# Kernel optimization log

Measured on AMD Instinct MI355X. Metric: run time of the kernel, lower is better.

The kernel has to match this reference:

```python
import jax, jax.numpy as jnp
import numpy as np

DIM = 512
HIDDEN = 1024
H2 = HIDDEN // 2
B = 384


def setup_inputs() -> dict:
    key = jax.random.key(0)
    ks = jax.random.split(key, 10)
    s_in = 1.0 / np.sqrt(DIM)
    s_h = 1.0 / np.sqrt(H2)
    return {
        "x_samples": jax.random.normal(ks[0], (B, DIM), dtype=jnp.float32),
        "y_samples": jax.random.normal(ks[1], (B, DIM), dtype=jnp.float32),
        "w1_mu": jax.random.uniform(ks[2], (DIM, H2), jnp.float32, -s_in, s_in),
        "b1_mu": jax.random.uniform(ks[3], (H2,), jnp.float32, -s_in, s_in),
        "w2_mu": jax.random.uniform(ks[4], (H2, DIM), jnp.float32, -s_h, s_h),
        "b2_mu": jax.random.uniform(ks[5], (DIM,), jnp.float32, -s_h, s_h),
        "w1_lv": jax.random.uniform(ks[6], (DIM, H2), jnp.float32, -s_in, s_in),
        "b1_lv": jax.random.uniform(ks[7], (H2,), jnp.float32, -s_in, s_in),
        "w2_lv": jax.random.uniform(ks[8], (H2, DIM), jnp.float32, -s_h, s_h),
        "b2_lv": jax.random.uniform(ks[9], (DIM,), jnp.float32, -s_h, s_h),
    }


def reference(x_samples, y_samples, w1_mu, b1_mu, w2_mu, b2_mu,
              w1_lv, b1_lv, w2_lv, b2_lv):
    batch_size = y_samples.shape[0]
    # p_mu / p_logvar MLPs
    mu = jax.nn.relu(x_samples @ w1_mu + b1_mu) @ w2_mu + b2_mu           # [B, D]
    logvar = jnp.tanh(jax.nn.relu(x_samples @ w1_lv + b1_lv) @ w2_lv + b2_lv)  # [B, D]
    inv_var = jnp.exp(-logvar)

    # positive log-likelihood per sample
    positive = (-(mu - y_samples) ** 2 * 0.5 * inv_var - logvar * 0.5).sum(-1)  # [B]

    # pairwise Gaussian log-likelihoods: all_probs[i, j] = log N(y_j; mu_i)
    diff = y_samples[None, :, :] - mu[:, None, :]                          # [B, B, D]
    all_probs = (-diff ** 2 * 0.5 * inv_var[:, None, :]
                 - logvar[:, None, :] * 0.5).sum(-1)                       # [B, B]

    # faithful to the torch broadcast: [B,B] + [B,B,1] -> [B,B,B]
    diag_mask = jnp.eye(batch_size, dtype=jnp.float32)[:, :, None] * -20.0  # [B, B, 1]
    scores = all_probs + diag_mask                                         # [B, B, B]
    negative = jax.scipy.special.logsumexp(scores, axis=0) - jnp.log(batch_size - 1.0)  # [B, B]

    upper = (positive - negative).mean()

    loglikeli = (-(mu - y_samples) ** 2 * inv_var - logvar).sum(1).mean(0)
    return loglikeli + jax.lax.stop_gradient(-loglikeli + upper)
```

## Files before the change

### kernel.cpp

```cpp
#include <hip/hip_runtime.h>
#include <math.h>

#define DIM  512
#define H2   512
#define BSZ  384



template<bool RELU>
__device__ __forceinline__ void gemm_tile(
    const float* __restrict__ A, const float* __restrict__ B,
    const float* __restrict__ bias, float* __restrict__ C,
    int m0, int n0,
    float (*As)[34], float (*Bs)[64])
{
    const int tid = threadIdx.x;
    const int tx = tid & 15;
    const int ty = tid >> 4;

    const int r_a  = tid >> 3;
    const int kg_a = tid & 7;
    const int kr_b = tid >> 4;
    const int cg_b = tid & 15;

    float acc[2][4] = {};

    float4 a_pf  = *(const float4*)&A[(size_t)(m0 + r_a) * 512 + kg_a * 4];
    float4 b_pf0 = *(const float4*)&B[(size_t)kr_b        * 512 + n0 + cg_b * 4];
    float4 b_pf1 = *(const float4*)&B[(size_t)(kr_b + 16) * 512 + n0 + cg_b * 4];

    for (int it = 0; it < 16; ++it) {
        __syncthreads();
        {
            float av[4];
            *(float4*)av = a_pf;
            #pragma unroll
            for (int j = 0; j < 4; ++j) As[kg_a * 4 + j][r_a] = av[j];
            *(float4*)&Bs[kr_b][cg_b * 4]      = b_pf0;
            *(float4*)&Bs[kr_b + 16][cg_b * 4] = b_pf1;
        }
        __syncthreads();

        if (it < 15) {
            const int k0n = (it + 1) * 32;
            a_pf  = *(const float4*)&A[(size_t)(m0 + r_a) * 512 + k0n + kg_a * 4];
            b_pf0 = *(const float4*)&B[(size_t)(k0n + kr_b)      * 512 + n0 + cg_b * 4];
            b_pf1 = *(const float4*)&B[(size_t)(k0n + kr_b + 16) * 512 + n0 + cg_b * 4];
        }

        #pragma unroll
        for (int kk = 0; kk < 32; ++kk) {
            const float a0 = As[kk][ty * 2 + 0];
            const float a1 = As[kk][ty * 2 + 1];
            const float4 bv = *(const float4*)&Bs[kk][tx * 4];
            acc[0][0] += a0 * bv.x; acc[0][1] += a0 * bv.y;
            acc[0][2] += a0 * bv.z; acc[0][3] += a0 * bv.w;
            acc[1][0] += a1 * bv.x; acc[1][1] += a1 * bv.y;
            acc[1][2] += a1 * bv.z; acc[1][3] += a1 * bv.w;
        }
    }

    float bb[4] = {0.f, 0.f, 0.f, 0.f};
    if (RELU) *(float4*)bb = *(const float4*)&bias[n0 + tx * 4];
    #pragma unroll
    for (int i = 0; i < 2; ++i) {
        float4 o;
        if (RELU) {
            o.x = fmaxf(acc[i][0] + bb[0], 0.f);
            o.y = fmaxf(acc[i][1] + bb[1], 0.f);
            o.z = fmaxf(acc[i][2] + bb[2], 0.f);
            o.w = fmaxf(acc[i][3] + bb[3], 0.f);
        } else {
            o.x = acc[i][0]; o.y = acc[i][1]; o.z = acc[i][2]; o.w = acc[i][3];
        }
        *(float4*)&C[(size_t)(m0 + ty * 2 + i) * 512 + n0 + tx * 4] = o;
    }
}

__global__ __launch_bounds__(256) void k_layer1(
    const float* __restrict__ x,
    const float* __restrict__ w1mu, const float* __restrict__ b1mu,
    const float* __restrict__ w1lv, const float* __restrict__ b1lv,
    const float* __restrict__ y,
    float* __restrict__ hmu, float* __restrict__ hlv,
    float* __restrict__ m1p, float* __restrict__ m2p)
{
    __shared__ float As[32][34];
    __shared__ float Bs[32][64];

    const int b = blockIdx.x;
    const int tid = threadIdx.x;

    if (b >= 192) {
        __shared__ float r1[2][512];
        __shared__ float r2[2][512];
        const int sb = b - 192;
        const int c4 = tid & 127;
        const int rh = tid >> 7;
        const int r0 = sb * 64 + rh * 32;
        float s1[4] = {0.f, 0.f, 0.f, 0.f};
        float s2[4] = {0.f, 0.f, 0.f, 0.f};
        for (int r = 0; r < 32; ++r) {
            float v[4];
            *(float4*)v = *(const float4*)&y[(size_t)(r0 + r) * 512 + c4 * 4];
            #pragma unroll
            for (int j = 0; j < 4; ++j) { s1[j] += v[j]; s2[j] += v[j] * v[j]; }
        }
        #pragma unroll
        for (int j = 0; j < 4; ++j) { r1[rh][c4 * 4 + j] = s1[j]; r2[rh][c4 * 4 + j] = s2[j]; }
        __syncthreads();
        if (rh == 0) {
            float4 o1, o2;
            o1.x = s1[0] + r1[1][c4 * 4 + 0]; o1.y = s1[1] + r1[1][c4 * 4 + 1];
            o1.z = s1[2] + r1[1][c4 * 4 + 2]; o1.w = s1[3] + r1[1][c4 * 4 + 3];
            o2.x = s2[0] + r2[1][c4 * 4 + 0]; o2.y = s2[1] + r2[1][c4 * 4 + 1];
            o2.z = s2[2] + r2[1][c4 * 4 + 2]; o2.w = s2[3] + r2[1][c4 * 4 + 3];
            *(float4*)&m1p[sb * 512 + c4 * 4] = o1;
            *(float4*)&m2p[sb * 512 + c4 * 4] = o2;
        }
        return;
    }

    const int branch = b >> 7 >= 1 ? 1 : (b >= 96 ? 1 : 0);
    const int idx = branch ? b - 96 : b;
    const int m0 = (idx >> 3) * 32;
    const int n0 = (idx & 7) * 64;

    if (branch == 0)
        gemm_tile<true>(x, w1mu, b1mu, hmu, m0, n0, As, Bs);
    else
        gemm_tile<true>(x, w1lv, b1lv, hlv, m0, n0, As, Bs);
}

__global__ __launch_bounds__(256) void k_layer2(
    const float* __restrict__ hmu, const float* __restrict__ hlv,
    const float* __restrict__ w2mu, const float* __restrict__ w2lv,
    float* __restrict__ gmu, float* __restrict__ glv)
{
    __shared__ float As[32][34];
    __shared__ float Bs[32][64];

    const int b = blockIdx.x;
    const int branch = b >= 96 ? 1 : 0;
    const int idx = branch ? b - 96 : b;
    const int m0 = (idx >> 3) * 32;
    const int n0 = (idx & 7) * 64;

    if (branch == 0)
        gemm_tile<false>(hmu, w2mu, nullptr, gmu, m0, n0, As, Bs);
    else
        gemm_tile<false>(hlv, w2lv, nullptr, glv, m0, n0, As, Bs);
}

__global__ __launch_bounds__(256) void k_epilogue(
    const float* __restrict__ gmu, const float* __restrict__ glv,
    const float* __restrict__ b2mu, const float* __restrict__ b2lv,
    const float* __restrict__ y,
    const float* __restrict__ m1p, const float* __restrict__ m2p,
    double* __restrict__ partials)
{
    __shared__ double wsum[4];
    const int tid = threadIdx.x;
    const float inv_b = 1.0f / (float)BSZ;

    float tsum = 0.f;
    #pragma unroll
    for (int jj = 0; jj < 2; ++jj) {
        const int e4 = blockIdx.x * 512 + tid * 2 + jj;
        const int col4 = e4 & 127;
        const size_t off = (size_t)e4 * 4;

        float gm[4], gl[4], yv[4], bm[4], bl[4], s1[4], s2[4];
        *(float4*)gm = *(const float4*)&gmu[off];
        *(float4*)gl = *(const float4*)&glv[off];
        *(float4*)yv = *(const float4*)&y[off];
        *(float4*)bm = *(const float4*)&b2mu[col4 * 4];
        *(float4*)bl = *(const float4*)&b2lv[col4 * 4];
        #pragma unroll
        for (int j = 0; j < 4; ++j) { s1[j] = 0.f; s2[j] = 0.f; }
        #pragma unroll
        for (int t = 0; t < 6; ++t) {
            float p1[4], p2[4];
            *(float4*)p1 = *(const float4*)&m1p[t * 512 + col4 * 4];
            *(float4*)p2 = *(const float4*)&m2p[t * 512 + col4 * 4];
            #pragma unroll
            for (int j = 0; j < 4; ++j) { s1[j] += p1[j]; s2[j] += p2[j]; }
        }
        #pragma unroll
        for (int j = 0; j < 4; ++j) {
            const float m1 = s1[j] * inv_b;
            const float m2 = s2[j] * inv_b;
            const float mu = gm[j] + bm[j];
            const float lv = tanhf(gl[j] + bl[j]);
            const float iv = expf(-lv);
            tsum += iv * ((yv[j] * yv[j] - m2) + 2.f * mu * (m1 - yv[j]));
        }
    }

    float s = tsum;
    #pragma unroll
    for (int off = 32; off > 0; off >>= 1) s += __shfl_down(s, off);
    if ((tid & 63) == 0) wsum[tid >> 6] = (double)s;
    __syncthreads();
    if (tid == 0)
        partials[blockIdx.x] = wsum[0] + wsum[1] + wsum[2] + wsum[3];
}

__global__ void k_final(const double* __restrict__ partials, float* __restrict__ out)
{
    const int t = threadIdx.x;
    double v = partials[t] + (t < 32 ? partials[64 + t] : 0.0);
    #pragma unroll
    for (int off = 32; off > 0; off >>= 1) v += __shfl_down(v, off);
    if (t == 0) {
        const double C0 = 5.381602146862063e-12;
        out[0] = (float)(-0.5 * v / (double)BSZ - C0);
    }
}

extern "C" void kernel_launch(void* const* d_in, const int* in_sizes, int n_in,
                              void* d_out, int out_size, void* d_ws, size_t ws_size,
                              hipStream_t stream) {
    const float* x    = (const float*)d_in[0];
    const float* y    = (const float*)d_in[1];
    const float* w1mu = (const float*)d_in[2];
    const float* b1mu = (const float*)d_in[3];
    const float* w2mu = (const float*)d_in[4];
    const float* b2mu = (const float*)d_in[5];
    const float* w1lv = (const float*)d_in[6];
    const float* b1lv = (const float*)d_in[7];
    const float* w2lv = (const float*)d_in[8];
    const float* b2lv = (const float*)d_in[9];
    float* out = (float*)d_out;

    float* ws = (float*)d_ws;
    float* hmu = ws;
    float* hlv = ws + 196608;
    float* gmu = ws + 393216;
    float* glv = ws + 589824;
    float* m1p = ws + 786432;
    float* m2p = ws + 789504;
    double* partials = (double*)(ws + 792576);

    k_layer1<<<198, 256, 0, stream>>>(x, w1mu, b1mu, w1lv, b1lv, y,
                                      hmu, hlv, m1p, m2p);
    k_layer2<<<192, 256, 0, stream>>>(hmu, hlv, w2mu, w2lv, gmu, glv);
    k_epilogue<<<96, 256, 0, stream>>>(gmu, glv, b2mu, b2lv, y, m1p, m2p, partials);
    k_final<<<1, 64, 0, stream>>>(partials, out);
}
```

Measured before the change: 111.8 us.

## Split GEMM K-dimension across blocks and fuse final reduction into epilogue

Both MLP GEMMs now split the K dimension into two halves computed by separate blocks, which doubles the grid to 384 blocks of 128 threads, each producing a 32x64 tile with a 4x4 register tile. The partial results are combined downstream. Layer 2 sums the two layer-1 partials, adds the bias and applies ReLU when loading A, and the epilogue sums the two layer-2 partials. The separate final-reduction kernel is replaced by an atomic counter so the last epilogue block does the reduction, removing one launch. The cost is extra workspace traffic for the partial buffers and a counter reset inside layer1.

```diff
diff --git a/kernel.cpp b/kernel.cpp
--- a/kernel.cpp
+++ b/kernel.cpp
@@ -1,220 +1,238 @@
 #include <hip/hip_runtime.h>
 #include <math.h>
 
-#define DIM  512
-#define H2   512
-#define BSZ  384
-
-
-
-template<bool RELU>
-__device__ __forceinline__ void gemm_tile(
-    const float* __restrict__ A, const float* __restrict__ B,
-    const float* __restrict__ bias, float* __restrict__ C,
-    int m0, int n0,
-    float (*As)[34], float (*Bs)[64])
-{
-    const int tid = threadIdx.x;
-    const int tx = tid & 15;
-    const int ty = tid >> 4;
-
-    const int r_a  = tid >> 3;
-    const int kg_a = tid & 7;
-    const int kr_b = tid >> 4;
-    const int cg_b = tid & 15;
-
-    float acc[2][4] = {};
-
-    float4 a_pf  = *(const float4*)&A[(size_t)(m0 + r_a) * 512 + kg_a * 4];
-    float4 b_pf0 = *(const float4*)&B[(size_t)kr_b        * 512 + n0 + cg_b * 4];
-    float4 b_pf1 = *(const float4*)&B[(size_t)(kr_b + 16) * 512 + n0 + cg_b * 4];
-
-    for (int it = 0; it < 16; ++it) {
+#define NROW 384
+#define NCOL 512
+
+#define HP_OFF   0
+#define GP_OFF   786432
+#define M1_OFF   1572864
+#define M2_OFF   1575936
+#define PART_OFF 1579008
+#define CNT_OFF  1579392
+
+template<bool COMBINE>
+__device__ __forceinline__ void gemm32x64(
+    const float* __restrict__ A0, const float* __restrict__ A1,
+    const float* __restrict__ bias1,
+    const float* __restrict__ W, float* __restrict__ C,
+    int m0, int n0, int ca)
+{
+    __shared__ __align__(16) float As[32][34];
+    __shared__ __align__(16) float Bs[32][64];
+
+    const int t  = threadIdx.x;
+    const int tx = t & 15;
+    const int ty = t >> 4;
+    const int r_a = t >> 3;
+    const int kg  = (t & 7) * 4;
+    const int kr  = t >> 4;
+    const int cg  = (t & 15) * 4;
+
+    float4 a_pf0, a_pf1, c_pf0, c_pf1, bb_pf;
+    float4 b_pf[4];
+
+    auto load_iter = [&](int k0) {
+        const float* a0p = &A0[(size_t)(m0 + r_a) * NCOL + ca + k0 + kg];
+        a_pf0 = *(const float4*)a0p;
+        a_pf1 = *(const float4*)(a0p + 16 * NCOL);
+        if (COMBINE) {
+            const float* a1p = &A1[(size_t)(m0 + r_a) * NCOL + ca + k0 + kg];
+            c_pf0 = *(const float4*)a1p;
+            c_pf1 = *(const float4*)(a1p + 16 * NCOL);
+            bb_pf = *(const float4*)&bias1[ca + k0 + kg];
+        }
+        #pragma unroll
+        for (int i = 0; i < 4; ++i)
+            b_pf[i] = *(const float4*)&W[(size_t)(ca + k0 + kr + 8 * i) * NCOL + n0 + cg];
+    };
+
+    float acc[4][4] = {};
+    load_iter(0);
+
+    for (int it = 0; it < 8; ++it) {
         __syncthreads();
         {
-            float av[4];
-            *(float4*)av = a_pf;
-            #pragma unroll
-            for (int j = 0; j < 4; ++j) As[kg_a * 4 + j][r_a] = av[j];
-            *(float4*)&Bs[kr_b][cg_b * 4]      = b_pf0;
-            *(float4*)&Bs[kr_b + 16][cg_b * 4] = b_pf1;
+            float av0[4], av1[4];
+            *(float4*)av0 = a_pf0; *(float4*)av1 = a_pf1;
+            if (COMBINE) {
+                float cv0[4], cv1[4], bv[4];
+                *(float4*)cv0 = c_pf0; *(float4*)cv1 = c_pf1;
+                *(float4*)bv  = bb_pf;
+                #pragma unroll
+                for (int j = 0; j < 4; ++j) {
+                    av0[j] = fmaxf(av0[j] + cv0[j] + bv[j], 0.f);
+                    av1[j] = fmaxf(av1[j] + cv1[j] + bv[j], 0.f);
+                }
+            }
+            #pragma unroll
+            for (int j = 0; j < 4; ++j) {
+                As[kg + j][r_a]      = av0[j];
+                As[kg + j][r_a + 16] = av1[j];
+            }
+            #pragma unroll
+            for (int i = 0; i < 4; ++i)
+                *(float4*)&Bs[kr + 8 * i][cg] = b_pf[i];
         }
         __syncthreads();
-
-        if (it < 15) {
-            const int k0n = (it + 1) * 32;
-            a_pf  = *(const float4*)&A[(size_t)(m0 + r_a) * 512 + k0n + kg_a * 4];
-            b_pf0 = *(const float4*)&B[(size_t)(k0n + kr_b)      * 512 + n0 + cg_b * 4];
-            b_pf1 = *(const float4*)&B[(size_t)(k0n + kr_b + 16) * 512 + n0 + cg_b * 4];
-        }
+        if (it < 7) load_iter((it + 1) * 32);
 
         #pragma unroll
         for (int kk = 0; kk < 32; ++kk) {
-            const float a0 = As[kk][ty * 2 + 0];
-            const float a1 = As[kk][ty * 2 + 1];
-            const float4 bv = *(const float4*)&Bs[kk][tx * 4];
-            acc[0][0] += a0 * bv.x; acc[0][1] += a0 * bv.y;
-            acc[0][2] += a0 * bv.z; acc[0][3] += a0 * bv.w;
-            acc[1][0] += a1 * bv.x; acc[1][1] += a1 * bv.y;
-            acc[1][2] += a1 * bv.z; acc[1][3] += a1 * bv.w;
-        }
-    }
-
-    float bb[4] = {0.f, 0.f, 0.f, 0.f};
-    if (RELU) *(float4*)bb = *(const float4*)&bias[n0 + tx * 4];
-    #pragma unroll
-    for (int i = 0; i < 2; ++i) {
-        float4 o;
-        if (RELU) {
-            o.x = fmaxf(acc[i][0] + bb[0], 0.f);
-            o.y = fmaxf(acc[i][1] + bb[1], 0.f);
-            o.z = fmaxf(acc[i][2] + bb[2], 0.f);
-            o.w = fmaxf(acc[i][3] + bb[3], 0.f);
-        } else {
-            o.x = acc[i][0]; o.y = acc[i][1]; o.z = acc[i][2]; o.w = acc[i][3];
-        }
-        *(float4*)&C[(size_t)(m0 + ty * 2 + i) * 512 + n0 + tx * 4] = o;
-    }
-}
-
-__global__ __launch_bounds__(256) void k_layer1(
+            float av[4], bv[4];
+            *(float2*)&av[0] = *(const float2*)&As[kk][ty * 4];
+            *(float2*)&av[2] = *(const float2*)&As[kk][ty * 4 + 2];
+            *(float4*)bv     = *(const float4*)&Bs[kk][tx * 4];
+            #pragma unroll
+            for (int i = 0; i < 4; ++i) {
+                acc[i][0] += av[i] * bv[0];
+                acc[i][1] += av[i] * bv[1];
+                acc[i][2] += av[i] * bv[2];
+                acc[i][3] += av[i] * bv[3];
+            }
+        }
+    }
+
+    #pragma unroll
+    for (int i = 0; i < 4; ++i) {
+        float4 o = make_float4(acc[i][0], acc[i][1], acc[i][2], acc[i][3]);
+        *(float4*)&C[(size_t)(m0 + ty * 4 + i) * NCOL + n0 + tx * 4] = o;
+    }
+}
+
+__global__ __launch_bounds__(128, 2) void k_layer1(
     const float* __restrict__ x,
-    const float* __restrict__ w1mu, const float* __restrict__ b1mu,
-    const float* __restrict__ w1lv, const float* __restrict__ b1lv,
-    const float* __restrict__ y,
-    float* __restrict__ hmu, float* __restrict__ hlv,
-    float* __restrict__ m1p, float* __restrict__ m2p)
-{
-    __shared__ float As[32][34];
-    __shared__ float Bs[32][64];
-
+    const float* __restrict__ w1mu, const float* __restrict__ w1lv,
+    const float* __restrict__ y, float* __restrict__ ws)
+{
     const int b = blockIdx.x;
-    const int tid = threadIdx.x;
-
-    if (b >= 192) {
-        __shared__ float r1[2][512];
-        __shared__ float r2[2][512];
-        const int sb = b - 192;
-        const int c4 = tid & 127;
-        const int rh = tid >> 7;
-        const int r0 = sb * 64 + rh * 32;
+    const int t = threadIdx.x;
+
+    if (b == 0 && t == 0) *(int*)(ws + CNT_OFF) = 0;
+
+    if (b >= 384) {
+        const int sb = b - 384;
+        const int c  = t * 4;
         float s1[4] = {0.f, 0.f, 0.f, 0.f};
         float s2[4] = {0.f, 0.f, 0.f, 0.f};
-        for (int r = 0; r < 32; ++r) {
+        #pragma unroll 4
+        for (int r = 0; r < 64; ++r) {
             float v[4];
-            *(float4*)v = *(const float4*)&y[(size_t)(r0 + r) * 512 + c4 * 4];
+            *(float4*)v = *(const float4*)&y[(size_t)(sb * 64 + r) * NCOL + c];
             #pragma unroll
             for (int j = 0; j < 4; ++j) { s1[j] += v[j]; s2[j] += v[j] * v[j]; }
         }
-        #pragma unroll
-        for (int j = 0; j < 4; ++j) { r1[rh][c4 * 4 + j] = s1[j]; r2[rh][c4 * 4 + j] = s2[j]; }
-        __syncthreads();
-        if (rh == 0) {
-            float4 o1, o2;
-            o1.x = s1[0] + r1[1][c4 * 4 + 0]; o1.y = s1[1] + r1[1][c4 * 4 + 1];
-            o1.z = s1[2] + r1[1][c4 * 4 + 2]; o1.w = s1[3] + r1[1][c4 * 4 + 3];
-            o2.x = s2[0] + r2[1][c4 * 4 + 0]; o2.y = s2[1] + r2[1][c4 * 4 + 1];
-            o2.z = s2[2] + r2[1][c4 * 4 + 2]; o2.w = s2[3] + r2[1][c4 * 4 + 3];
-            *(float4*)&m1p[sb * 512 + c4 * 4] = o1;
-            *(float4*)&m2p[sb * 512 + c4 * 4] = o2;
-        }
+        *(float4*)&ws[M1_OFF + sb * NCOL + c] = make_float4(s1[0], s1[1], s1[2], s1[3]);
+        *(float4*)&ws[M2_OFF + sb * NCOL + c] = make_float4(s2[0], s2[1], s2[2], s2[3]);
         return;
     }
 
-    const int branch = b >> 7 >= 1 ? 1 : (b >= 96 ? 1 : 0);
-    const int idx = branch ? b - 96 : b;
-    const int m0 = (idx >> 3) * 32;
-    const int n0 = (idx & 7) * 64;
-
-    if (branch == 0)
-        gemm_tile<true>(x, w1mu, b1mu, hmu, m0, n0, As, Bs);
-    else
-        gemm_tile<true>(x, w1lv, b1lv, hlv, m0, n0, As, Bs);
-}
-
-__global__ __launch_bounds__(256) void k_layer2(
-    const float* __restrict__ hmu, const float* __restrict__ hlv,
-    const float* __restrict__ w2mu, const float* __restrict__ w2lv,
-    float* __restrict__ gmu, float* __restrict__ glv)
-{
-    __shared__ float As[32][34];
-    __shared__ float Bs[32][64];
-
+    const int branch = b / 192;
+    const int rem    = b % 192;
+    const int sl     = rem / 96;
+    const int mt     = (rem % 96) >> 3;
+    const int nt     = rem & 7;
+
+    const float* W = branch ? w1lv : w1mu;
+    float* C = ws + HP_OFF + (size_t)(branch * 2 + sl) * 196608;
+    gemm32x64<false>(x, nullptr, nullptr, W, C, mt * 32, nt * 64, sl * 256);
+}
+
+__global__ __launch_bounds__(128, 2) void k_layer2(
+    const float* __restrict__ w2mu, const float* __restrict__ b1mu,
+    const float* __restrict__ w2lv, const float* __restrict__ b1lv,
+    float* __restrict__ ws)
+{
     const int b = blockIdx.x;
-    const int branch = b >= 96 ? 1 : 0;
-    const int idx = branch ? b - 96 : b;
-    const int m0 = (idx >> 3) * 32;
-    const int n0 = (idx & 7) * 64;
-
-    if (branch == 0)
-        gemm_tile<false>(hmu, w2mu, nullptr, gmu, m0, n0, As, Bs);
-    else
-        gemm_tile<false>(hlv, w2lv, nullptr, glv, m0, n0, As, Bs);
+    const int branch = b / 192;
+    const int rem    = b % 192;
+    const int sl     = rem / 96;
+    const int mt     = (rem % 96) >> 3;
+    const int nt     = rem & 7;
+
+    const float* A0 = ws + HP_OFF + (size_t)(branch * 2 + 0) * 196608;
+    const float* A1 = ws + HP_OFF + (size_t)(branch * 2 + 1) * 196608;
+    const float* bias1 = branch ? b1lv : b1mu;
+    const float* W = branch ? w2lv : w2mu;
+    float* C = ws + GP_OFF + (size_t)(branch * 2 + sl) * 196608;
+    gemm32x64<true>(A0, A1, bias1, W, C, mt * 32, nt * 64, sl * 256);
 }
 
 __global__ __launch_bounds__(256) void k_epilogue(
-    const float* __restrict__ gmu, const float* __restrict__ glv,
     const float* __restrict__ b2mu, const float* __restrict__ b2lv,
-    const float* __restrict__ y,
-    const float* __restrict__ m1p, const float* __restrict__ m2p,
-    double* __restrict__ partials)
+    const float* __restrict__ y, float* __restrict__ ws,
+    float* __restrict__ out)
 {
     __shared__ double wsum[4];
-    const int tid = threadIdx.x;
-    const float inv_b = 1.0f / (float)BSZ;
+    __shared__ int is_last;
+
+    const int t = threadIdx.x;
+    const float inv_b = 1.0f / (float)NROW;
+
+    const int e4   = blockIdx.x * 256 + t;
+    const int col4 = e4 & 127;
+    const size_t off = (size_t)e4 * 4;
+
+    const float* gm0 = ws + GP_OFF;
+    const float* gm1 = ws + GP_OFF + 196608;
+    const float* gl0 = ws + GP_OFF + 2 * 196608;
+    const float* gl1 = ws + GP_OFF + 3 * 196608;
+
+    float gm[4], gq[4], gl[4], gr[4], yv[4], bm[4], bl[4], s1[4], s2[4];
+    *(float4*)gm = *(const float4*)&gm0[off];
+    *(float4*)gq = *(const float4*)&gm1[off];
+    *(float4*)gl = *(const float4*)&gl0[off];
+    *(float4*)gr = *(const float4*)&gl1[off];
+    *(float4*)yv = *(const float4*)&y[off];
+    *(float4*)bm = *(const float4*)&b2mu[col4 * 4];
+    *(float4*)bl = *(const float4*)&b2lv[col4 * 4];
+    #pragma unroll
+    for (int j = 0; j < 4; ++j) { s1[j] = 0.f; s2[j] = 0.f; }
+    #pragma unroll
+    for (int p = 0; p < 6; ++p) {
+        float p1[4], p2[4];
+        *(float4*)p1 = *(const float4*)&ws[M1_OFF + p * NCOL + col4 * 4];
+        *(float4*)p2 = *(const float4*)&ws[M2_OFF + p * NCOL + col4 * 4];
+        #pragma unroll
+        for (int j = 0; j < 4; ++j) { s1[j] += p1[j]; s2[j] += p2[j]; }
+    }
 
     float tsum = 0.f;
     #pragma unroll
-    for (int jj = 0; jj < 2; ++jj) {
-        const int e4 = blockIdx.x * 512 + tid * 2 + jj;
-        const int col4 = e4 & 127;
-        const size_t off = (size_t)e4 * 4;
-
-        float gm[4], gl[4], yv[4], bm[4], bl[4], s1[4], s2[4];
-        *(float4*)gm = *(const float4*)&gmu[off];
-        *(float4*)gl = *(const float4*)&glv[off];
-        *(float4*)yv = *(const float4*)&y[off];
-        *(float4*)bm = *(const float4*)&b2mu[col4 * 4];
-        *(float4*)bl = *(const float4*)&b2lv[col4 * 4];
-        #pragma unroll
-        for (int j = 0; j < 4; ++j) { s1[j] = 0.f; s2[j] = 0.f; }
-        #pragma unroll
-        for (int t = 0; t < 6; ++t) {
-            float p1[4], p2[4];
-            *(float4*)p1 = *(const float4*)&m1p[t * 512 + col4 * 4];
-            *(float4*)p2 = *(const float4*)&m2p[t * 512 + col4 * 4];
-            #pragma unroll
-            for (int j = 0; j < 4; ++j) { s1[j] += p1[j]; s2[j] += p2[j]; }
-        }
-        #pragma unroll
-        for (int j = 0; j < 4; ++j) {
-            const float m1 = s1[j] * inv_b;
-            const float m2 = s2[j] * inv_b;
-            const float mu = gm[j] + bm[j];
-            const float lv = tanhf(gl[j] + bl[j]);
-            const float iv = expf(-lv);
-            tsum += iv * ((yv[j] * yv[j] - m2) + 2.f * mu * (m1 - yv[j]));
-        }
+    for (int j = 0; j < 4; ++j) {
+        const float m1 = s1[j] * inv_b;
+        const float m2 = s2[j] * inv_b;
+        const float mu = gm[j] + gq[j] + bm[j];
+        const float lv = tanhf(gl[j] + gr[j] + bl[j]);
+        const float iv = expf(-lv);
+        tsum += iv * ((yv[j] * yv[j] - m2) + 2.f * mu * (m1 - yv[j]));
     }
 
     float s = tsum;
     #pragma unroll
-    for (int off = 32; off > 0; off >>= 1) s += __shfl_down(s, off);
-    if ((tid & 63) == 0) wsum[tid >> 6] = (double)s;
+    for (int o = 32; o > 0; o >>= 1) s += __shfl_down(s, o);
+    if ((t & 63) == 0) wsum[t >> 6] = (double)s;
     __syncthreads();
-    if (tid == 0)
+
+    double* partials = (double*)(ws + PART_OFF);
+    int* counter = (int*)(ws + CNT_OFF);
+    if (t == 0) {
         partials[blockIdx.x] = wsum[0] + wsum[1] + wsum[2] + wsum[3];
-}
-
-__global__ void k_final(const double* __restrict__ partials, float* __restrict__ out)
-{
-    const int t = threadIdx.x;
-    double v = partials[t] + (t < 32 ? partials[64 + t] : 0.0);
-    #pragma unroll
-    for (int off = 32; off > 0; off >>= 1) v += __shfl_down(v, off);
-    if (t == 0) {
-        const double C0 = 5.381602146862063e-12;
-        out[0] = (float)(-0.5 * v / (double)BSZ - C0);
+        __threadfence();
+        const int old = atomicAdd(counter, 1);
+        is_last = (old == 191) ? 1 : 0;
+    }
+    __syncthreads();
+
+    if (is_last && t < 64) {
+        __threadfence();
+        double v = partials[t] + partials[t + 64] + partials[t + 128];
+        #pragma unroll
+        for (int o = 32; o > 0; o >>= 1) v += __shfl_down(v, o);
+        if (t == 0) {
+            const double C0 = 5.381602146862063e-12;
+            out[0] = (float)(-0.5 * v / (double)NROW - C0);
+        }
     }
 }
 
@@ -232,19 +250,9 @@
     const float* w2lv = (const float*)d_in[8];
     const float* b2lv = (const float*)d_in[9];
     float* out = (float*)d_out;
-
-    float* ws = (float*)d_ws;
-    float* hmu = ws;
-    float* hlv = ws + 196608;
-    float* gmu = ws + 393216;
-    float* glv = ws + 589824;
-    float* m1p = ws + 786432;
-    float* m2p = ws + 789504;
-    double* partials = (double*)(ws + 792576);
-
-    k_layer1<<<198, 256, 0, stream>>>(x, w1mu, b1mu, w1lv, b1lv, y,
-                                      hmu, hlv, m1p, m2p);
-    k_layer2<<<192, 256, 0, stream>>>(hmu, hlv, w2mu, w2lv, gmu, glv);
-    k_epilogue<<<96, 256, 0, stream>>>(gmu, glv, b2mu, b2lv, y, m1p, m2p, partials);
-    k_final<<<1, 64, 0, stream>>>(partials, out);
-}
+    float* ws  = (float*)d_ws;
+
+    k_layer1<<<390, 128, 0, stream>>>(x, w1mu, w1lv, y, ws);
+    k_layer2<<<384, 128, 0, stream>>>(w2mu, b1mu, w2lv, b1lv, ws);
+    k_epilogue<<<192, 256, 0, stream>>>(b2mu, b2lv, y, ws, out);
+}
```

Result: slower. 118.5 us (+6.0%).
